# Performance work log

Measured on AMD Instinct MI355X. Metric: run time of the kernel, lower is better.

Reference implementation:

```python
import jax, jax.numpy as jnp
import numpy as np

N = 30000      # nodes
E = 480000     # edges (before self loops)
NFEAT = 128
H = 16         # heads
C = 32         # per-head channels = nhid
NCLASS = 10
G = 64         # graphs in batch
ATT_SLOPE = 0.2   # GATv2Conv negative_slope default
ACT_SLOPE = 0.01  # F.leaky_relu default


def setup_inputs() -> dict:
    key = jax.random.key(0)
    ks = jax.random.split(key, 16)
    def glorot(k, shape):
        fan = sum(shape[:2]) if len(shape) > 1 else shape[0]
        return jax.random.normal(k, shape, jnp.float32) * (2.0 / fan) ** 0.5
    inp = {
        "x": jax.random.normal(ks[0], (N, NFEAT), jnp.float32),
        # layer 1: lin_l / lin_r map NFEAT -> H*C, attention vector att [H, C]
        "Wl1": glorot(ks[1], (NFEAT, H * C)), "bl1": jnp.zeros((H * C,), jnp.float32),
        "Wr1": glorot(ks[2], (NFEAT, H * C)), "br1": jnp.zeros((H * C,), jnp.float32),
        "att1": glorot(ks[3], (H, C)), "b1": jnp.zeros((C,), jnp.float32),
        # layer 2: nhid(=C) -> H*C
        "Wl2": glorot(ks[4], (C, H * C)), "bl2": jnp.zeros((H * C,), jnp.float32),
        "Wr2": glorot(ks[5], (C, H * C)), "br2": jnp.zeros((H * C,), jnp.float32),
        "att2": glorot(ks[6], (H, C)), "b2": jnp.zeros((C,), jnp.float32),
        # classifier nhid -> nclass
        "Wc": glorot(ks[7], (C, NCLASS)), "bc": jnp.zeros((NCLASS,), jnp.float32),
        "edge_index": jax.random.randint(ks[8], (2, E), 0, N, jnp.int32),
        "batch": jnp.sort(jax.random.randint(ks[9], (N,), 0, G, jnp.int32)),
    }
    return inp


def _gatv2_layer(x, Wl, bl, Wr, br, att, b, src, dst, n):
    # GATv2Conv, concat=False (mean over heads), eval mode (no dropout)
    xl = (x @ Wl + bl).reshape(n, H, C)   # messages (x_j)
    xr = (x @ Wr + br).reshape(n, H, C)   # query side (x_i)
    e = jax.nn.leaky_relu(xl[src] + xr[dst], ATT_SLOPE)      # [E', H, C]
    score = jnp.einsum('ehc,hc->eh', e, att)                 # [E', H]
    # segment softmax over incoming edges of each dst node
    m = jax.ops.segment_max(score, dst, num_segments=n)
    ex = jnp.exp(score - m[dst])
    denom = jax.ops.segment_sum(ex, dst, num_segments=n)
    alpha = ex / denom[dst]                                  # [E', H]
    out = jax.ops.segment_sum(alpha[:, :, None] * xl[src], dst, num_segments=n)
    return out.mean(axis=1) + b                              # [n, C]


def reference(x, Wl1, bl1, Wr1, br1, att1, b1, Wl2, bl2, Wr2, br2, att2, b2, Wc, bc, edge_index, batch):
    # add self loops (PyG GATv2Conv default add_self_loops=True)
    loop = jnp.arange(N, dtype=edge_index.dtype)
    src = jnp.concatenate([edge_index[0], loop])
    dst = jnp.concatenate([edge_index[1], loop])

    h = jax.nn.leaky_relu(_gatv2_layer(x, Wl1, bl1, Wr1, br1, att1, b1, src, dst, N), ACT_SLOPE)
    h = jax.nn.leaky_relu(_gatv2_layer(h, Wl2, bl2, Wr2, br2, att2, b2, src, dst, N), ACT_SLOPE)
    # dropout is identity in eval mode
    # global mean pool over graphs
    summed = jax.ops.segment_sum(h, batch, num_segments=G)               # [G, C]
    counts = jax.ops.segment_sum(jnp.ones((N,), h.dtype), batch, num_segments=G)
    pooled = summed / jnp.maximum(counts, 1.0)[:, None]
    logits = pooled @ Wc + bc
    return logits / 1.0  # temperature = 1.0
```

## Files before the change

### kernel.cpp

```cpp
#include <hip/hip_runtime.h>
#include <float.h>

#define NNODES 30000
#define NEDGES 480000
#define NFEATK 128
#define NH 16
#define NC 32
#define HC 512
#define NCLASSES 10
#define NG 64
#define CAP 96

using half2v = __attribute__((ext_vector_type(2))) _Float16;
using half4 = __attribute__((ext_vector_type(4))) _Float16;
using half8 = __attribute__((ext_vector_type(8))) _Float16;
using f32x4 = __attribute__((ext_vector_type(4))) float;

__global__ void prep0_kernel(const float* __restrict__ x, _Float16* __restrict__ xh,
                             const float* __restrict__ Wl1, const float* __restrict__ Wr1,
                             _Float16* __restrict__ Wlt1, _Float16* __restrict__ Wrt1,
                             const float* __restrict__ Wl2, const float* __restrict__ Wr2,
                             _Float16* __restrict__ Wlt2, _Float16* __restrict__ Wrt2,
                             int* __restrict__ cnt, unsigned short* __restrict__ csr) {
    int gtid = blockIdx.x * blockDim.x + threadIdx.x;
    int gstride = gridDim.x * blockDim.x;
    for (int i = gtid; i < NNODES * NFEATK / 4; i += gstride) {
        float4 v = *(const float4*)&x[i * 4];
        half4 h = {(_Float16)v.x, (_Float16)v.y, (_Float16)v.z, (_Float16)v.w};
        *(half4*)&xh[i * 4] = h;
    }
    for (int i = gtid; i < 2 * 512 * NFEATK; i += gstride) {
        int sel = i >= 512 * NFEATK;
        int idx = i - sel * 512 * NFEATK;
        const float* W = sel ? Wr1 : Wl1;
        _Float16* Wt = sel ? Wrt1 : Wlt1;
        int n = idx & 511, k = idx >> 9;
        Wt[n * NFEATK + k] = (_Float16)W[idx];
    }
    for (int i = gtid; i < 2 * 512 * NC; i += gstride) {
        int sel = i >= 512 * NC;
        int idx = i - sel * 512 * NC;
        const float* W = sel ? Wr2 : Wl2;
        _Float16* Wt = sel ? Wrt2 : Wlt2;
        int n = idx & 511, k = idx >> 9;
        Wt[n * NC + k] = (_Float16)W[idx];
    }
    for (int i = gtid; i < NNODES; i += gstride) {
        cnt[i] = 1;
        csr[i * CAP] = (unsigned short)i;
    }
}

__global__ void scatter_kernel(const int* __restrict__ src, const int* __restrict__ dst,
                               int* __restrict__ cnt, unsigned short* __restrict__ csr) {
    int e = blockIdx.x * blockDim.x + threadIdx.x;
    if (e >= NEDGES) return;
    int s = src[e], d = dst[e];
    int pos = atomicAdd(&cnt[d], 1);
    csr[d * CAP + pos] = (unsigned short)s;
}

template <int K>
__launch_bounds__(256)
__global__ void dual_gemm_kernel(const _Float16* __restrict__ A,
                                 const _Float16* __restrict__ Wlt, const _Float16* __restrict__ Wrt,
                                 const float* __restrict__ bl, const float* __restrict__ br,
                                 _Float16* __restrict__ Yl, _Float16* __restrict__ Yr) {
    constexpr int KS = (K > 64) ? 64 : K;
    constexpr int KcS = KS / 8;
    constexpr int AH = 64 * KS;
    constexpr int BH = 128 * KS;
    constexpr int YSH = 64 * 136;
    constexpr int SMEMH = (AH + BH > YSH) ? (AH + BH) : YSH;
    __shared__ __align__(16) _Float16 smem[SMEMH];
    _Float16* as = smem;
    _Float16* bs = smem + AH;

    int tid = threadIdx.x;
    int sel = blockIdx.x >> 2;
    int nbase = (blockIdx.x & 3) * 128;
    const _Float16* Bt = sel ? Wrt : Wlt;
    const float* bias = sel ? br : bl;
    _Float16* Y = sel ? Yr : Yl;
    int mb = blockIdx.y;

    int wave = tid >> 6, lane = tid & 63;
    int quad = lane >> 4, l16 = lane & 15;
    int am = l16 & (KcS - 1);

    f32x4 acc[8];
    #pragma unroll
    for (int f = 0; f < 8; f++) acc[f] = (f32x4){0.f, 0.f, 0.f, 0.f};

    #pragma unroll
    for (int ko = 0; ko < K / KS; ++ko) {
        if (ko) __syncthreads();
        for (int c = tid; c < 64 * KcS; c += 256) {
            int row = c / KcS, k8 = c % KcS;
            int arow = mb * 64 + row; if (arow > NNODES - 1) arow = NNODES - 1;
            half8 v = *(const half8*)&A[(size_t)arow * K + (ko * KcS + k8) * 8];
            *(half8*)&as[(row * KcS + (k8 ^ (row & (KcS - 1)))) * 8] = v;
        }
        for (int c = tid; c < 128 * KcS; c += 256) {
            int row = c / KcS, k8 = c % KcS;
            half8 v = *(const half8*)&Bt[(size_t)(nbase + row) * K + (ko * KcS + k8) * 8];
            *(half8*)&bs[(row * KcS + (k8 ^ (row & (KcS - 1)))) * 8] = v;
        }
        __syncthreads();

        #pragma unroll
        for (int kk = 0; kk < KcS; kk += 4) {
            int k8 = (kk + quad) ^ am;
            half8 a = *(const half8*)&as[((wave * 16 + l16) * KcS + k8) * 8];
            #pragma unroll
            for (int f = 0; f < 8; f++) {
                half8 b = *(const half8*)&bs[((f * 16 + l16) * KcS + k8) * 8];
                acc[f] = __builtin_amdgcn_mfma_f32_16x16x32_f16(a, b, acc[f], 0, 0, 0);
            }
        }
    }
    __syncthreads();

    _Float16* ys = smem;
    #pragma unroll
    for (int f = 0; f < 8; f++) {
        float bv = bias[nbase + f * 16 + l16];
        #pragma unroll
        for (int r = 0; r < 4; r++) {
            ys[(wave * 16 + quad * 4 + r) * 136 + f * 16 + l16] = (_Float16)(acc[f][r] + bv);
        }
    }
    __syncthreads();
    int mtop = mb * 64;
    for (int c = tid; c < 64 * 16; c += 256) {
        int r = c >> 4, cc = (c & 15) * 8;
        int grow = mtop + r;
        if (grow < NNODES)
            *(half8*)&Y[(size_t)grow * HC + nbase + cc] = *(half8*)&ys[r * 136 + cc];
    }
}

__device__ inline half2v lrelu2(half2v e) {
    half2v s = e * half2v{(_Float16)0.2f, (_Float16)0.2f};
    return __builtin_elementwise_max(e, s);
}

#if __has_builtin(__builtin_amdgcn_fdot2)
#define FDOT2(a, b, c) __builtin_amdgcn_fdot2((a), (b), (c), false)
#else
__device__ inline float fdot2_sw(half2v a, half2v b, float c) {
    half2v p = a * b;
    return c + (float)p.x + (float)p.y;
}
#define FDOT2(a, b, c) fdot2_sw((a), (b), (c))
#endif

template <typename OUT>
__launch_bounds__(256)
__global__ void gat_edge_kernel(const _Float16* __restrict__ xlh, const _Float16* __restrict__ xrh,
                                const float* __restrict__ att, const float* __restrict__ bvec,
                                const int* __restrict__ cnt, const unsigned short* __restrict__ csr_src,
                                OUT* __restrict__ hout) {
    int wv = threadIdx.x >> 6;
    int t = threadIdx.x & 63;
    int d = blockIdx.x * 4 + wv;
    int col = t * 8;

    half8 xrq = *(const half8*)&xrh[(unsigned)d * HC + col];
    half2v xr0 = {xrq[0], xrq[1]}, xr1 = {xrq[2], xrq[3]};
    half2v xr2 = {xrq[4], xrq[5]}, xr3 = {xrq[6], xrq[7]};
    float4 atta = *(const float4*)&att[col];
    float4 attb = *(const float4*)&att[col + 4];
    half2v at0 = {(_Float16)atta.x, (_Float16)atta.y};
    half2v at1 = {(_Float16)atta.z, (_Float16)atta.w};
    half2v at2 = {(_Float16)attb.x, (_Float16)attb.y};
    half2v at3 = {(_Float16)attb.z, (_Float16)attb.w};

    int beg = d * CAP, end = beg + cnt[d];

    float l = 0.f;
    float a[8];
    #pragma unroll
    for (int c = 0; c < 8; c++) a[c] = 0.f;

    for (int i = beg; i < end; i += 4) {
        int n = end - i;
        int s0 = csr_src[i];
        int s1 = csr_src[n > 1 ? i + 1 : i];
        int s2 = csr_src[n > 2 ? i + 2 : i];
        int s3 = csr_src[n > 3 ? i + 3 : i];
        half8 q0 = *(const half8*)&xlh[(unsigned)s0 * HC + col];
        half8 q1 = *(const half8*)&xlh[(unsigned)s1 * HC + col];
        half8 q2 = *(const half8*)&xlh[(unsigned)s2 * HC + col];
        half8 q3 = *(const half8*)&xlh[(unsigned)s3 * HC + col];

        float v0 = 0.f, v1 = 0.f, v2 = 0.f, v3 = 0.f;
        v0 = FDOT2(lrelu2(half2v{q0[0], q0[1]} + xr0), at0, v0);
        v0 = FDOT2(lrelu2(half2v{q0[2], q0[3]} + xr1), at1, v0);
        v0 = FDOT2(lrelu2(half2v{q0[4], q0[5]} + xr2), at2, v0);
        v0 = FDOT2(lrelu2(half2v{q0[6], q0[7]} + xr3), at3, v0);
        v1 = FDOT2(lrelu2(half2v{q1[0], q1[1]} + xr0), at0, v1);
        v1 = FDOT2(lrelu2(half2v{q1[2], q1[3]} + xr1), at1, v1);
        v1 = FDOT2(lrelu2(half2v{q1[4], q1[5]} + xr2), at2, v1);
        v1 = FDOT2(lrelu2(half2v{q1[6], q1[7]} + xr3), at3, v1);
        v2 = FDOT2(lrelu2(half2v{q2[0], q2[1]} + xr0), at0, v2);
        v2 = FDOT2(lrelu2(half2v{q2[2], q2[3]} + xr1), at1, v2);
        v2 = FDOT2(lrelu2(half2v{q2[4], q2[5]} + xr2), at2, v2);
        v2 = FDOT2(lrelu2(half2v{q2[6], q2[7]} + xr3), at3, v2);
        v3 = FDOT2(lrelu2(half2v{q3[0], q3[1]} + xr0), at0, v3);
        v3 = FDOT2(lrelu2(half2v{q3[2], q3[3]} + xr1), at1, v3);
        v3 = FDOT2(lrelu2(half2v{q3[4], q3[5]} + xr2), at2, v3);
        v3 = FDOT2(lrelu2(half2v{q3[6], q3[7]} + xr3), at3, v3);

        v0 += __shfl_xor(v0, 1); v1 += __shfl_xor(v1, 1);
        v2 += __shfl_xor(v2, 1); v3 += __shfl_xor(v3, 1);
        v0 += __shfl_xor(v0, 2); v1 += __shfl_xor(v1, 2);
        v2 += __shfl_xor(v2, 2); v3 += __shfl_xor(v3, 2);

        float p0 = __expf(v0);
        float p1 = (n > 1) ? __expf(v1) : 0.f;
        float p2 = (n > 2) ? __expf(v2) : 0.f;
        float p3 = (n > 3) ? __expf(v3) : 0.f;
        l += (p0 + p1) + (p2 + p3);

        #pragma unroll
        for (int c = 0; c < 8; c++) {
            a[c] += p0 * (float)q0[c];
            a[c] += p1 * (float)q1[c];
            a[c] += p2 * (float)q2[c];
            a[c] += p3 * (float)q3[c];
        }
    }

    float inv = 1.0f / l;
    #pragma unroll
    for (int c = 0; c < 8; c++) a[c] *= inv;

    #pragma unroll
    for (int off = 4; off < 64; off <<= 1) {
        #pragma unroll
        for (int c = 0; c < 8; c++) a[c] += __shfl_xor(a[c], off);
    }

    if (t < 4) {
        #pragma unroll
        for (int c = 0; c < 8; c++) {
            float r = a[c] * (1.0f / (float)NH) + bvec[t * 8 + c];
            r = (r > 0.f) ? r : 0.01f * r;
            hout[(size_t)d * NC + t * 8 + c] = (OUT)r;
        }
    }
}

__launch_bounds__(1024)
__global__ void pool_classify_kernel(const float* __restrict__ h, const int* __restrict__ batch,
                                     const float* __restrict__ Wc, const float* __restrict__ bc,
                                     float* __restrict__ out) {
    int g = blockIdx.x;
    int lo = 0, hi = NNODES;
    while (lo < hi) { int mid = (lo + hi) >> 1; if (batch[mid] < g) lo = mid + 1; else hi = mid; }
    int start = lo;
    hi = NNODES;
    while (lo < hi) { int mid = (lo + hi) >> 1; if (batch[mid] <= g) lo = mid + 1; else hi = mid; }
    int endn = lo;
    int cntg = endn - start;

    int tid = threadIdx.x;
    int c = tid & 31, nl = tid >> 5;
    float s = 0.f;
    for (int n = start + nl; n < endn; n += 32) s += h[n * NC + c];
    __shared__ float red[1024];
    red[tid] = s;
    __syncthreads();
    if (tid < 32) {
        float t = 0.f;
        #pragma unroll
        for (int j = 0; j < 32; j++) t += red[j * 32 + tid];
        red[tid] = t / fmaxf((float)cntg, 1.0f);
    }
    __syncthreads();
    if (tid < NCLASSES) {
        float sum = bc[tid];
        #pragma unroll
        for (int cc = 0; cc < NC; cc++) sum += red[cc] * Wc[cc * NCLASSES + tid];
        out[g * NCLASSES + tid] = sum;
    }
}


extern "C" void kernel_launch(void* const* d_in, const int* in_sizes, int n_in,
                              void* d_out, int out_size, void* d_ws, size_t ws_size,
                              hipStream_t stream) {
    const float* x    = (const float*)d_in[0];
    const float* Wl1  = (const float*)d_in[1];
    const float* bl1  = (const float*)d_in[2];
    const float* Wr1  = (const float*)d_in[3];
    const float* br1  = (const float*)d_in[4];
    const float* att1 = (const float*)d_in[5];
    const float* b1   = (const float*)d_in[6];
    const float* Wl2  = (const float*)d_in[7];
    const float* bl2  = (const float*)d_in[8];
    const float* Wr2  = (const float*)d_in[9];
    const float* br2  = (const float*)d_in[10];
    const float* att2 = (const float*)d_in[11];
    const float* b2   = (const float*)d_in[12];
    const float* Wc   = (const float*)d_in[13];
    const float* bc   = (const float*)d_in[14];
    const int* ei     = (const int*)d_in[15];
    const int* batch  = (const int*)d_in[16];
    float* out = (float*)d_out;

    const int* srcp = ei;
    const int* dstp = ei + NEDGES;

    char* ws = (char*)d_ws;
    size_t off = 0;
    auto alloc = [&](size_t bytes) -> void* {
        void* p = ws + off;
        off += (bytes + 255) & ~(size_t)255;
        return p;
    };
    _Float16* xlh  = (_Float16*)alloc(sizeof(_Float16) * (size_t)NNODES * HC);
    _Float16* xrh  = (_Float16*)alloc(sizeof(_Float16) * (size_t)NNODES * HC);
    _Float16* xh   = (_Float16*)alloc(sizeof(_Float16) * (size_t)NNODES * NFEATK);
    _Float16* h1   = (_Float16*)alloc(sizeof(_Float16) * (size_t)NNODES * NC);
    float* h2      = (float*)alloc(sizeof(float) * (size_t)NNODES * NC);
    _Float16* Wlt1 = (_Float16*)alloc(sizeof(_Float16) * 512 * NFEATK);
    _Float16* Wrt1 = (_Float16*)alloc(sizeof(_Float16) * 512 * NFEATK);
    _Float16* Wlt2 = (_Float16*)alloc(sizeof(_Float16) * 512 * NC);
    _Float16* Wrt2 = (_Float16*)alloc(sizeof(_Float16) * 512 * NC);
    int*   cnt     = (int*)alloc(sizeof(int) * NNODES);
    unsigned short* csr = (unsigned short*)alloc(sizeof(unsigned short) * (size_t)NNODES * CAP);

    prep0_kernel<<<512, 256, 0, stream>>>(x, xh, Wl1, Wr1, Wlt1, Wrt1,
                                          Wl2, Wr2, Wlt2, Wrt2, cnt, csr);
    scatter_kernel<<<(NEDGES + 255) / 256, 256, 0, stream>>>(srcp, dstp, cnt, csr);

    const int MB = (NNODES + 63) / 64;

    dual_gemm_kernel<NFEATK><<<dim3(8, MB), 256, 0, stream>>>(xh, Wlt1, Wrt1, bl1, br1, xlh, xrh);
    gat_edge_kernel<_Float16><<<NNODES / 4, 256, 0, stream>>>(xlh, xrh, att1, b1, cnt, csr, h1);

    dual_gemm_kernel<NC><<<dim3(8, MB), 256, 0, stream>>>(h1, Wlt2, Wrt2, bl2, br2, xlh, xrh);
    gat_edge_kernel<float><<<NNODES / 4, 256, 0, stream>>>(xlh, xrh, att2, b2, cnt, csr, h2);

    pool_classify_kernel<<<NG, 1024, 0, stream>>>(h2, batch, Wc, bc, out);
}
```

Before: 319.8 us.

## Fuse fp32-to-fp16 input conversion into GEMM, share A tile, unroll edge loop

The separate pass that converts x to fp16 is removed, and the layer-1 GEMM now reads fp32 x and converts it while loading the tile. Each GEMM block now computes both the left and right projections from one shared A tile, which halves the grid and the A reloads at the cost of twice the accumulator registers and more shared memory. The edge aggregation loop processes 8 neighbors per iteration instead of 4, giving more loads in flight but using more registers. Together these aim to cut memory traffic and kernel count, with some risk of lower occupancy.

After: 357.3 us. 11.7% more time.

```diff
diff --git a/kernel.cpp b/kernel.cpp
--- a/kernel.cpp
+++ b/kernel.cpp
@@ -16,19 +16,13 @@
 using half8 = __attribute__((ext_vector_type(8))) _Float16;
 using f32x4 = __attribute__((ext_vector_type(4))) float;
 
-__global__ void prep0_kernel(const float* __restrict__ x, _Float16* __restrict__ xh,
-                             const float* __restrict__ Wl1, const float* __restrict__ Wr1,
+__global__ void prep0_kernel(const float* __restrict__ Wl1, const float* __restrict__ Wr1,
                              _Float16* __restrict__ Wlt1, _Float16* __restrict__ Wrt1,
                              const float* __restrict__ Wl2, const float* __restrict__ Wr2,
                              _Float16* __restrict__ Wlt2, _Float16* __restrict__ Wrt2,
                              int* __restrict__ cnt, unsigned short* __restrict__ csr) {
     int gtid = blockIdx.x * blockDim.x + threadIdx.x;
     int gstride = gridDim.x * blockDim.x;
-    for (int i = gtid; i < NNODES * NFEATK / 4; i += gstride) {
-        float4 v = *(const float4*)&x[i * 4];
-        half4 h = {(_Float16)v.x, (_Float16)v.y, (_Float16)v.z, (_Float16)v.w};
-        *(half4*)&xh[i * 4] = h;
-    }
     for (int i = gtid; i < 2 * 512 * NFEATK; i += gstride) {
         int sel = i >= 512 * NFEATK;
         int idx = i - sel * 512 * NFEATK;
@@ -60,9 +54,9 @@
     csr[d * CAP + pos] = (unsigned short)s;
 }
 
-template <int K>
+template <int K, typename AT>
 __launch_bounds__(256)
-__global__ void dual_gemm_kernel(const _Float16* __restrict__ A,
+__global__ void dual_gemm_kernel(const AT* __restrict__ A,
                                  const _Float16* __restrict__ Wlt, const _Float16* __restrict__ Wrt,
                                  const float* __restrict__ bl, const float* __restrict__ br,
                                  _Float16* __restrict__ Yl, _Float16* __restrict__ Yr) {
@@ -71,26 +65,26 @@
     constexpr int AH = 64 * KS;
     constexpr int BH = 128 * KS;
     constexpr int YSH = 64 * 136;
-    constexpr int SMEMH = (AH + BH > YSH) ? (AH + BH) : YSH;
+    constexpr int SMEMH = (AH + 2 * BH > YSH) ? (AH + 2 * BH) : YSH;
     __shared__ __align__(16) _Float16 smem[SMEMH];
     _Float16* as = smem;
-    _Float16* bs = smem + AH;
+    _Float16* bsl = smem + AH;
+    _Float16* bsr = smem + AH + BH;
 
     int tid = threadIdx.x;
-    int sel = blockIdx.x >> 2;
-    int nbase = (blockIdx.x & 3) * 128;
-    const _Float16* Bt = sel ? Wrt : Wlt;
-    const float* bias = sel ? br : bl;
-    _Float16* Y = sel ? Yr : Yl;
+    int nbase = blockIdx.x * 128;
     int mb = blockIdx.y;
 
     int wave = tid >> 6, lane = tid & 63;
     int quad = lane >> 4, l16 = lane & 15;
     int am = l16 & (KcS - 1);
 
-    f32x4 acc[8];
-    #pragma unroll
-    for (int f = 0; f < 8; f++) acc[f] = (f32x4){0.f, 0.f, 0.f, 0.f};
+    f32x4 accl[8], accr[8];
+    #pragma unroll
+    for (int f = 0; f < 8; f++) {
+        accl[f] = (f32x4){0.f, 0.f, 0.f, 0.f};
+        accr[f] = (f32x4){0.f, 0.f, 0.f, 0.f};
+    }
 
     #pragma unroll
     for (int ko = 0; ko < K / KS; ++ko) {
@@ -98,11 +92,24 @@
         for (int c = tid; c < 64 * KcS; c += 256) {
             int row = c / KcS, k8 = c % KcS;
             int arow = mb * 64 + row; if (arow > NNODES - 1) arow = NNODES - 1;
-            half8 v = *(const half8*)&A[(size_t)arow * K + (ko * KcS + k8) * 8];
+            half8 v;
+            if constexpr (sizeof(AT) == 4) {
+                const float* ap = (const float*)&A[(size_t)arow * K + (ko * KcS + k8) * 8];
+                float4 f0 = *(const float4*)ap;
+                float4 f1 = *(const float4*)(ap + 4);
+                v = half8{(_Float16)f0.x, (_Float16)f0.y, (_Float16)f0.z, (_Float16)f0.w,
+                          (_Float16)f1.x, (_Float16)f1.y, (_Float16)f1.z, (_Float16)f1.w};
+            } else {
+                v = *(const half8*)&A[(size_t)arow * K + (ko * KcS + k8) * 8];
+            }
             *(half8*)&as[(row * KcS + (k8 ^ (row & (KcS - 1)))) * 8] = v;
         }
-        for (int c = tid; c < 128 * KcS; c += 256) {
-            int row = c / KcS, k8 = c % KcS;
+        for (int c = tid; c < 2 * 128 * KcS; c += 256) {
+            int sel = c >= 128 * KcS;
+            int cc = c - sel * 128 * KcS;
+            int row = cc / KcS, k8 = cc % KcS;
+            const _Float16* Bt = sel ? Wrt : Wlt;
+            _Float16* bs = sel ? bsr : bsl;
             half8 v = *(const half8*)&Bt[(size_t)(nbase + row) * K + (ko * KcS + k8) * 8];
             *(half8*)&bs[(row * KcS + (k8 ^ (row & (KcS - 1)))) * 8] = v;
         }
@@ -114,29 +121,48 @@
             half8 a = *(const half8*)&as[((wave * 16 + l16) * KcS + k8) * 8];
             #pragma unroll
             for (int f = 0; f < 8; f++) {
-                half8 b = *(const half8*)&bs[((f * 16 + l16) * KcS + k8) * 8];
-                acc[f] = __builtin_amdgcn_mfma_f32_16x16x32_f16(a, b, acc[f], 0, 0, 0);
+                half8 b = *(const half8*)&bsl[((f * 16 + l16) * KcS + k8) * 8];
+                accl[f] = __builtin_amdgcn_mfma_f32_16x16x32_f16(a, b, accl[f], 0, 0, 0);
             }
+            #pragma unroll
+            for (int f = 0; f < 8; f++) {
+                half8 b = *(const half8*)&bsr[((f * 16 + l16) * KcS + k8) * 8];
+                accr[f] = __builtin_amdgcn_mfma_f32_16x16x32_f16(a, b, accr[f], 0, 0, 0);
+            }
         }
     }
     __syncthreads();
 
     _Float16* ys = smem;
+    int mtop = mb * 64;
     #pragma unroll
     for (int f = 0; f < 8; f++) {
-        float bv = bias[nbase + f * 16 + l16];
-        #pragma unroll
-        for (int r = 0; r < 4; r++) {
-            ys[(wave * 16 + quad * 4 + r) * 136 + f * 16 + l16] = (_Float16)(acc[f][r] + bv);
-        }
-    }
-    __syncthreads();
-    int mtop = mb * 64;
+        float bv = bl[nbase + f * 16 + l16];
+        #pragma unroll
+        for (int r = 0; r < 4; r++)
+            ys[(wave * 16 + quad * 4 + r) * 136 + f * 16 + l16] = (_Float16)(accl[f][r] + bv);
+    }
+    __syncthreads();
     for (int c = tid; c < 64 * 16; c += 256) {
         int r = c >> 4, cc = (c & 15) * 8;
         int grow = mtop + r;
         if (grow < NNODES)
-            *(half8*)&Y[(size_t)grow * HC + nbase + cc] = *(half8*)&ys[r * 136 + cc];
+            *(half8*)&Yl[(size_t)grow * HC + nbase + cc] = *(half8*)&ys[r * 136 + cc];
+    }
+    __syncthreads();
+    #pragma unroll
+    for (int f = 0; f < 8; f++) {
+        float bv = br[nbase + f * 16 + l16];
+        #pragma unroll
+        for (int r = 0; r < 4; r++)
+            ys[(wave * 16 + quad * 4 + r) * 136 + f * 16 + l16] = (_Float16)(accr[f][r] + bv);
+    }
+    __syncthreads();
+    for (int c = tid; c < 64 * 16; c += 256) {
+        int r = c >> 4, cc = (c & 15) * 8;
+        int grow = mtop + r;
+        if (grow < NNODES)
+            *(half8*)&Yr[(size_t)grow * HC + nbase + cc] = *(half8*)&ys[r * 136 + cc];
     }
 }
 
@@ -183,52 +209,33 @@
     #pragma unroll
     for (int c = 0; c < 8; c++) a[c] = 0.f;
 
-    for (int i = beg; i < end; i += 4) {
+    for (int i = beg; i < end; i += 8) {
         int n = end - i;
-        int s0 = csr_src[i];
-        int s1 = csr_src[n > 1 ? i + 1 : i];
-        int s2 = csr_src[n > 2 ? i + 2 : i];
-        int s3 = csr_src[n > 3 ? i + 3 : i];
-        half8 q0 = *(const half8*)&xlh[(unsigned)s0 * HC + col];
-        half8 q1 = *(const half8*)&xlh[(unsigned)s1 * HC + col];
-        half8 q2 = *(const half8*)&xlh[(unsigned)s2 * HC + col];
-        half8 q3 = *(const half8*)&xlh[(unsigned)s3 * HC + col];
-
-        float v0 = 0.f, v1 = 0.f, v2 = 0.f, v3 = 0.f;
-        v0 = FDOT2(lrelu2(half2v{q0[0], q0[1]} + xr0), at0, v0);
-        v0 = FDOT2(lrelu2(half2v{q0[2], q0[3]} + xr1), at1, v0);
-        v0 = FDOT2(lrelu2(half2v{q0[4], q0[5]} + xr2), at2, v0);
-        v0 = FDOT2(lrelu2(half2v{q0[6], q0[7]} + xr3), at3, v0);
-        v1 = FDOT2(lrelu2(half2v{q1[0], q1[1]} + xr0), at0, v1);
-        v1 = FDOT2(lrelu2(half2v{q1[2], q1[3]} + xr1), at1, v1);
-        v1 = FDOT2(lrelu2(half2v{q1[4], q1[5]} + xr2), at2, v1);
-        v1 = FDOT2(lrelu2(half2v{q1[6], q1[7]} + xr3), at3, v1);
-        v2 = FDOT2(lrelu2(half2v{q2[0], q2[1]} + xr0), at0, v2);
-        v2 = FDOT2(lrelu2(half2v{q2[2], q2[3]} + xr1), at1, v2);
-        v2 = FDOT2(lrelu2(half2v{q2[4], q2[5]} + xr2), at2, v2);
-        v2 = FDOT2(lrelu2(half2v{q2[6], q2[7]} + xr3), at3, v2);
-        v3 = FDOT2(lrelu2(half2v{q3[0], q3[1]} + xr0), at0, v3);
-        v3 = FDOT2(lrelu2(half2v{q3[2], q3[3]} + xr1), at1, v3);
-        v3 = FDOT2(lrelu2(half2v{q3[4], q3[5]} + xr2), at2, v3);
-        v3 = FDOT2(lrelu2(half2v{q3[6], q3[7]} + xr3), at3, v3);
-
-        v0 += __shfl_xor(v0, 1); v1 += __shfl_xor(v1, 1);
-        v2 += __shfl_xor(v2, 1); v3 += __shfl_xor(v3, 1);
-        v0 += __shfl_xor(v0, 2); v1 += __shfl_xor(v1, 2);
-        v2 += __shfl_xor(v2, 2); v3 += __shfl_xor(v3, 2);
-
-        float p0 = __expf(v0);
-        float p1 = (n > 1) ? __expf(v1) : 0.f;
-        float p2 = (n > 2) ? __expf(v2) : 0.f;
-        float p3 = (n > 3) ? __expf(v3) : 0.f;
-        l += (p0 + p1) + (p2 + p3);
-
-        #pragma unroll
-        for (int c = 0; c < 8; c++) {
-            a[c] += p0 * (float)q0[c];
-            a[c] += p1 * (float)q1[c];
-            a[c] += p2 * (float)q2[c];
-            a[c] += p3 * (float)q3[c];
+        int sx[8];
+        #pragma unroll
+        for (int j = 0; j < 8; j++) sx[j] = csr_src[i + (j < n ? j : 0)];
+        half8 q[8];
+        #pragma unroll
+        for (int j = 0; j < 8; j++) q[j] = *(const half8*)&xlh[(unsigned)sx[j] * HC + col];
+
+        float v[8];
+        #pragma unroll
+        for (int j = 0; j < 8; j++) {
+            float vv = 0.f;
+            vv = FDOT2(lrelu2(half2v{q[j][0], q[j][1]} + xr0), at0, vv);
+            vv = FDOT2(lrelu2(half2v{q[j][2], q[j][3]} + xr1), at1, vv);
+            vv = FDOT2(lrelu2(half2v{q[j][4], q[j][5]} + xr2), at2, vv);
+            vv = FDOT2(lrelu2(half2v{q[j][6], q[j][7]} + xr3), at3, vv);
+            vv += __shfl_xor(vv, 1);
+            vv += __shfl_xor(vv, 2);
+            v[j] = vv;
+        }
+        #pragma unroll
+        for (int j = 0; j < 8; j++) {
+            float p = (j < n) ? __expf(v[j]) : 0.f;
+            l += p;
+            #pragma unroll
+            for (int c = 0; c < 8; c++) a[c] += p * (float)q[j][c];
         }
     }
 
@@ -322,7 +329,6 @@
     };
     _Float16* xlh  = (_Float16*)alloc(sizeof(_Float16) * (size_t)NNODES * HC);
     _Float16* xrh  = (_Float16*)alloc(sizeof(_Float16) * (size_t)NNODES * HC);
-    _Float16* xh   = (_Float16*)alloc(sizeof(_Float16) * (size_t)NNODES * NFEATK);
     _Float16* h1   = (_Float16*)alloc(sizeof(_Float16) * (size_t)NNODES * NC);
     float* h2      = (float*)alloc(sizeof(float) * (size_t)NNODES * NC);
     _Float16* Wlt1 = (_Float16*)alloc(sizeof(_Float16) * 512 * NFEATK);
@@ -332,16 +338,16 @@
     int*   cnt     = (int*)alloc(sizeof(int) * NNODES);
     unsigned short* csr = (unsigned short*)alloc(sizeof(unsigned short) * (size_t)NNODES * CAP);
 
-    prep0_kernel<<<512, 256, 0, stream>>>(x, xh, Wl1, Wr1, Wlt1, Wrt1,
+    prep0_kernel<<<256, 256, 0, stream>>>(Wl1, Wr1, Wlt1, Wrt1,
                                           Wl2, Wr2, Wlt2, Wrt2, cnt, csr);
     scatter_kernel<<<(NEDGES + 255) / 256, 256, 0, stream>>>(srcp, dstp, cnt, csr);
 
     const int MB = (NNODES + 63) / 64;
 
-    dual_gemm_kernel<NFEATK><<<dim3(8, MB), 256, 0, stream>>>(xh, Wlt1, Wrt1, bl1, br1, xlh, xrh);
+    dual_gemm_kernel<NFEATK, float><<<dim3(4, MB), 256, 0, stream>>>(x, Wlt1, Wrt1, bl1, br1, xlh, xrh);
     gat_edge_kernel<_Float16><<<NNODES / 4, 256, 0, stream>>>(xlh, xrh, att1, b1, cnt, csr, h1);
 
-    dual_gemm_kernel<NC><<<dim3(8, MB), 256, 0, stream>>>(h1, Wlt2, Wrt2, bl2, br2, xlh, xrh);
+    dual_gemm_kernel<NC, _Float16><<<dim3(4, MB), 256, 0, stream>>>(h1, Wlt2, Wrt2, bl2, br2, xlh, xrh);
     gat_edge_kernel<float><<<NNODES / 4, 256, 0, stream>>>(xlh, xrh, att2, b2, cnt, csr, h2);
 
     pool_classify_kernel<<<NG, 1024, 0, stream>>>(h2, batch, Wc, bc, out);
```
